# Optimization experiments

Hardware: AMD Instinct MI355X
Metric: run time of the kernel (lower is better)

Reference implementation:

```python
import jax, jax.numpy as jnp
import numpy as np

S, H, E, DFF = 8192, 1024, 8, 4096
CAPACITY = (S * 1) // E  # capacity_factor=1.0, k=1 -> 1024 (>= min_capacity 4)


def setup_inputs() -> dict:
    key = jax.random.key(0)
    ks = jax.random.split(key, 6)
    sc_in = 1.0 / np.sqrt(H)
    sc_ff = 1.0 / np.sqrt(DFF)
    return {
        "hidden_states": jax.random.normal(ks[0], (S, H), dtype=jnp.float32),
        "wg": jax.random.normal(ks[1], (H, E), dtype=jnp.float32) * sc_in,
        "w1": jax.random.normal(ks[2], (E, H, DFF), dtype=jnp.float32) * sc_in,
        "b1": jnp.zeros((E, DFF), dtype=jnp.float32),
        "w2": jax.random.normal(ks[3], (E, DFF, H), dtype=jnp.float32) * sc_ff,
        "b2": jnp.zeros((E, H), dtype=jnp.float32),
    }


def _top1_gate(x, wg):
    # DeepSpeed top1gating (noisy_gate_policy=None, used_token=None)
    logits = x @ wg                                   # [S, E]
    gates = jax.nn.softmax(logits, axis=-1)           # [S, E]
    idx = jnp.argmax(gates, axis=-1)                  # [S]
    mask1 = jax.nn.one_hot(idx, E, dtype=gates.dtype) # [S, E]
    # load-balancing aux loss (uses pre-capacity mask)
    me = jnp.mean(gates, axis=0)
    ce = jnp.mean(mask1, axis=0)
    l_aux = jnp.sum(me * ce) * E
    # capacity-based token dropping
    locations1 = jnp.cumsum(mask1, axis=0) - 1.0      # position within expert
    mask1 = mask1 * (locations1 < CAPACITY)
    exp_counts = jnp.sum(mask1, axis=0).astype(jnp.int32)
    loc_s = jnp.sum(locations1 * mask1, axis=1).astype(jnp.int32)   # [S]
    loc_sc = jax.nn.one_hot(loc_s, CAPACITY, dtype=gates.dtype)     # [S, C]
    combine = jnp.einsum("se,sc->sec", gates * mask1, loc_sc)       # [S, E, C]
    dispatch = (combine > 0).astype(gates.dtype)
    return l_aux, combine, dispatch, exp_counts


def reference(hidden_states, wg, w1, b1, w2, b2):
    l_aux, combine, dispatch, exp_counts = _top1_gate(hidden_states, wg)
    # dispatch tokens to expert slots: [E, C, H]
    disp = jnp.einsum("sec,sh->ech", dispatch, hidden_states)
    # grouped expert FFN (GELU MLP)
    h1 = jax.nn.gelu(jnp.einsum("ech,ehf->ecf", disp, w1) + b1[:, None, :])
    eo = jnp.einsum("ecf,efh->ech", h1, w2) + b2[:, None, :]
    # combine back to token order, weighted by gate values
    out = jnp.einsum("sec,ech->sh", combine, eo)      # [S, H]
    # dropout prob = 0.0 -> identity
    return out, l_aux, exp_counts
```

## Files before the change

### kernel.cpp

```cpp
#include <hip/hip_runtime.h>

#define S_TOK 8192
#define H_DIM 1024
#define NE    8
#define CAP   1024
#define DFF   4096

typedef unsigned short u16;
typedef __bf16 bf16_t;
typedef bf16_t bf16x8 __attribute__((ext_vector_type(8)));
typedef float  f32x4  __attribute__((ext_vector_type(4)));

__device__ __forceinline__ u16 f2bf(float f) {
  union { float f; unsigned u; } a; a.f = f;
  unsigned u = a.u;
  u += 0x7fffu + ((u >> 16) & 1u);
  return (u16)(u >> 16);
}

__device__ __forceinline__ float gelu_tanh(float x) {
  const float c = 0.7978845608028654f;
  float t = tanhf(c * (x + 0.044715f * x * x * x));
  return 0.5f * x * (1.0f + t);
}

__global__ void gate_kernel(const float* __restrict__ x, const float* __restrict__ wg,
                            float* __restrict__ gate, int* __restrict__ expert,
                            int* __restrict__ rank, int* __restrict__ blockCnt,
                            float* __restrict__ blockMe) {
  __shared__ float sg[16][8];
  __shared__ int   se[16];
  int tid = threadIdx.x, lane = tid & 63, w = tid >> 6;
  int b = blockIdx.x;
  for (int j = 0; j < 4; ++j) {
    int t = w * 4 + j;
    int s = b * 16 + t;
    const float* xr = x + (size_t)s * H_DIM;
    float acc[8];
#pragma unroll
    for (int e = 0; e < 8; ++e) acc[e] = 0.f;
#pragma unroll
    for (int i = 0; i < 16; ++i) {
      int h = i * 64 + lane;
      float xv = xr[h];
      float4 wa = *(const float4*)(wg + h * 8);
      float4 wb = *(const float4*)(wg + h * 8 + 4);
      acc[0] += xv * wa.x; acc[1] += xv * wa.y; acc[2] += xv * wa.z; acc[3] += xv * wa.w;
      acc[4] += xv * wb.x; acc[5] += xv * wb.y; acc[6] += xv * wb.z; acc[7] += xv * wb.w;
    }
#pragma unroll
    for (int off = 32; off >= 1; off >>= 1)
#pragma unroll
      for (int e = 0; e < 8; ++e) acc[e] += __shfl_down(acc[e], off);
    if (lane == 0) {
      float mx = acc[0];
#pragma unroll
      for (int e = 1; e < 8; ++e) mx = fmaxf(mx, acc[e]);
      float g[8], Z = 0.f;
#pragma unroll
      for (int e = 0; e < 8; ++e) { g[e] = expf(acc[e] - mx); Z += g[e]; }
      int am = 0; float best = acc[0];
#pragma unroll
      for (int e = 1; e < 8; ++e) if (acc[e] > best) { best = acc[e]; am = e; }
      float inv = 1.f / Z;
#pragma unroll
      for (int e = 0; e < 8; ++e) sg[t][e] = g[e] * inv;
      se[t] = am;
      gate[s] = g[am] * inv;
      expert[s] = am;
    }
  }
  __syncthreads();
  if (tid < 16) {
    int e = se[tid], r = 0;
    for (int t2 = 0; t2 < tid; ++t2) r += (se[t2] == e) ? 1 : 0;
    rank[b * 16 + tid] = r;
  }
  if (tid < 8) {
    int c = 0; float m = 0.f;
#pragma unroll
    for (int t = 0; t < 16; ++t) { c += (se[t] == tid) ? 1 : 0; m += sg[t][tid]; }
    blockCnt[b * 8 + tid] = c;
    blockMe[b * 8 + tid] = m;
  }
}

__global__ void scan_kernel(const int* __restrict__ blockCnt, const float* __restrict__ blockMe,
                            int* __restrict__ blockOff, int* __restrict__ counts,
                            float* __restrict__ tail) {
  int tid = threadIdx.x;
  int e = tid >> 6, lane = tid & 63;
  int run = 0; float msum = 0.f;
  for (int c = 0; c < 8; ++c) {
    int b = c * 64 + lane;
    int v = blockCnt[b * 8 + e];
    float mv = blockMe[b * 8 + e];
    int sc = v;
#pragma unroll
    for (int off = 1; off < 64; off <<= 1) {
      int u = __shfl_up(sc, off);
      if (lane >= off) sc += u;
    }
    blockOff[b * 8 + e] = run + sc - v;
    run += __shfl(sc, 63);
#pragma unroll
    for (int off = 32; off >= 1; off >>= 1) mv += __shfl_down(mv, off);
    msum += __shfl(mv, 0);
  }
  __shared__ float sm[8];
  __shared__ int scnt[8];
  if (lane == 0) {
    sm[e] = msum; scnt[e] = run;
    counts[e] = run < CAP ? run : CAP;
  }
  __syncthreads();
  if (tid == 0) {
    float la = 0.f;
    for (int i = 0; i < 8; ++i)
      la += (sm[i] / (float)S_TOK) * ((float)scnt[i] / (float)S_TOK);
    tail[0] = la * (float)NE;
    for (int i = 0; i < 8; ++i) {
      int cc = scnt[i] < CAP ? scnt[i] : CAP;
      tail[1 + i] = (float)cc;
    }
  }
}

__global__ void assign_kernel(const int* __restrict__ expert, const int* __restrict__ rank,
                              const int* __restrict__ blockOff, int* __restrict__ slot_token) {
  int s = blockIdx.x * 256 + threadIdx.x;
  int e = expert[s];
  int pos = blockOff[(s >> 4) * 8 + e] + rank[s];
  if (pos < CAP) slot_token[e * CAP + pos] = s;
}

__global__ void gather_kernel(const float* __restrict__ x, const int* __restrict__ slot_token,
                              const int* __restrict__ counts, u16* __restrict__ disp) {
  int slot = blockIdx.x;
  int e = slot >> 10, c = slot & 1023;
  int t = threadIdx.x;
  ushort4 v4;
  if (c < counts[e]) {
    int s = slot_token[slot];
    float4 v = *(const float4*)(x + (size_t)s * H_DIM + t * 4);
    v4.x = f2bf(v.x); v4.y = f2bf(v.y); v4.z = f2bf(v.z); v4.w = f2bf(v.w);
  } else {
    v4.x = 0; v4.y = 0; v4.z = 0; v4.w = 0;
  }
  *(ushort4*)(disp + (size_t)slot * H_DIM + t * 4) = v4;
}

__global__ void transpose_convert(const float* __restrict__ src0, u16* __restrict__ dst0,
                                  int R, int C) {
  __shared__ float tile[64][65];
  int e = blockIdx.z;
  const float* src = src0 + (size_t)e * R * C;
  u16* dst = dst0 + (size_t)e * R * C;
  int c0 = blockIdx.x * 64, r0 = blockIdx.y * 64;
  int g = threadIdx.x & 15, rr = threadIdx.x >> 4;
#pragma unroll
  for (int p = 0; p < 4; ++p) {
    int r = rr + p * 16;
    float4 v = *(const float4*)(src + (size_t)(r0 + r) * C + c0 + g * 4);
    tile[r][g * 4 + 0] = v.x;
    tile[r][g * 4 + 1] = v.y;
    tile[r][g * 4 + 2] = v.z;
    tile[r][g * 4 + 3] = v.w;
  }
  __syncthreads();
#pragma unroll
  for (int p = 0; p < 4; ++p) {
    int c = rr + p * 16;
    ushort4 o;
    o.x = f2bf(tile[g * 4 + 0][c]);
    o.y = f2bf(tile[g * 4 + 1][c]);
    o.z = f2bf(tile[g * 4 + 2][c]);
    o.w = f2bf(tile[g * 4 + 3][c]);
    *(ushort4*)(dst + (size_t)(c0 + c) * R + r0 + g * 4) = o;
  }
}

__device__ __forceinline__ void stage_tile(const u16* g, int ldk, u16* lds) {
  int tid = threadIdx.x;
  int lane = tid & 63, w = tid >> 6;
#pragma unroll
  for (int r = 0; r < 2; ++r) {
    int p = (w * 2 + r) * 64 + lane;
    int row = p >> 2;
    int kq = (p & 3) ^ ((row >> 1) & 3);
    const u16* gp = g + (size_t)row * ldk + kq * 8;
    u16* lp = lds + (w * 2 + r) * 512;
    __builtin_amdgcn_global_load_lds((__attribute__((address_space(1))) int*)(gp),
                                     (__attribute__((address_space(3))) int*)(lp),
                                     16, 0, 0);
  }
}

template <int KDIM>
__device__ __forceinline__ void gemm_core(const u16* A, const u16* Bt, int lda, int ldb,
                                          u16* As, u16* Bs, f32x4 acc[4][4]) {
  int tid = threadIdx.x;
  int lane = tid & 63;
  int w = tid >> 6, wm = w >> 1, wn = w & 1;
  int q = lane >> 4, l15 = lane & 15;
  int aoff[4], boff[4];
#pragma unroll
  for (int t = 0; t < 4; ++t) {
    int ra = wm * 64 + t * 16 + l15;
    aoff[t] = ra * 32 + ((q ^ ((ra >> 1) & 3)) * 8);
    int rb = wn * 64 + t * 16 + l15;
    boff[t] = rb * 32 + ((q ^ ((rb >> 1) & 3)) * 8);
  }
  for (int kt = 0; kt < KDIM; kt += 32) {
    stage_tile(A + kt, lda, As);
    stage_tile(Bt + kt, ldb, Bs);
    __syncthreads();
    bf16x8 af[4], bfr[4];
#pragma unroll
    for (int t = 0; t < 4; ++t) af[t] = *(const bf16x8*)(As + aoff[t]);
#pragma unroll
    for (int t = 0; t < 4; ++t) bfr[t] = *(const bf16x8*)(Bs + boff[t]);
#pragma unroll
    for (int mt = 0; mt < 4; ++mt)
#pragma unroll
      for (int nt = 0; nt < 4; ++nt)
        acc[mt][nt] = __builtin_amdgcn_mfma_f32_16x16x32_bf16(af[mt], bfr[nt], acc[mt][nt], 0, 0, 0);
    __syncthreads();
  }
}

__global__ __launch_bounds__(256, 2) void gemm1_kernel(const u16* __restrict__ disp,
                                                       const u16* __restrict__ w1t,
                                                       const float* __restrict__ b1,
                                                       u16* __restrict__ h1) {
  __shared__ __align__(16) u16 As[4096];
  __shared__ __align__(16) u16 Bs[4096];
  int e = blockIdx.z;
  int m0 = blockIdx.y * 128, n0 = blockIdx.x * 128;
  const u16* A  = disp + (size_t)e * CAP * H_DIM + (size_t)m0 * H_DIM;
  const u16* Bt = w1t + (size_t)e * DFF * H_DIM + (size_t)n0 * H_DIM;
  f32x4 acc[4][4];
  f32x4 zero = {0.f, 0.f, 0.f, 0.f};
#pragma unroll
  for (int i = 0; i < 4; ++i)
#pragma unroll
    for (int j = 0; j < 4; ++j) acc[i][j] = zero;
  gemm_core<H_DIM>(A, Bt, H_DIM, H_DIM, As, Bs, acc);
  int tid = threadIdx.x, lane = tid & 63, w = tid >> 6, wm = w >> 1, wn = w & 1;
  int q = lane >> 4, l15 = lane & 15;
  const float* b1e = b1 + e * DFF;
  u16* out = h1 + (size_t)e * CAP * DFF;
#pragma unroll
  for (int mt = 0; mt < 4; ++mt)
#pragma unroll
    for (int nt = 0; nt < 4; ++nt) {
      int col = n0 + wn * 64 + nt * 16 + l15;
      float bias = b1e[col];
#pragma unroll
      for (int r = 0; r < 4; ++r) {
        int row = m0 + wm * 64 + mt * 16 + q * 4 + r;
        out[(size_t)row * DFF + col] = f2bf(gelu_tanh(acc[mt][nt][r] + bias));
      }
    }
}

__global__ __launch_bounds__(512, 4) void gemm2_kernel(const u16* __restrict__ h1,
                                                       const u16* __restrict__ w2t,
                                                       const float* __restrict__ b2,
                                                       const int* __restrict__ slot_token,
                                                       const float* __restrict__ gate,
                                                       const int* __restrict__ counts,
                                                       float* __restrict__ out) {
  __shared__ __align__(16) u16 As[4096];
  __shared__ __align__(16) u16 Bs[4096];
  int e = blockIdx.z;
  int m0 = blockIdx.y * 128, n0 = blockIdx.x * 128;
  const u16* A  = h1 + (size_t)e * CAP * DFF + (size_t)m0 * DFF;
  const u16* Bt = w2t + (size_t)e * H_DIM * DFF + (size_t)n0 * DFF;
  int tid = threadIdx.x, lane = tid & 63, w = tid >> 6;
  int wm = w >> 2, wn = w & 3;
  int q = lane >> 4, l15 = lane & 15;
  f32x4 acc[4][2];
  f32x4 zero = {0.f, 0.f, 0.f, 0.f};
#pragma unroll
  for (int i = 0; i < 4; ++i) { acc[i][0] = zero; acc[i][1] = zero; }

  const u16* gsrc = (w < 4) ? A : Bt;
  u16* ldst = (w < 4) ? As : Bs;
  int q4 = w & 3;
  const u16* gp0[2]; u16* lp[2];
#pragma unroll
  for (int r = 0; r < 2; ++r) {
    int p = (q4 * 2 + r) * 64 + lane;
    int srow = p >> 2;
    int skq = (p & 3) ^ ((srow >> 1) & 3);
    gp0[r] = gsrc + (size_t)srow * DFF + skq * 8;
    lp[r] = ldst + (q4 * 2 + r) * 512;
  }

  int aoff[4], boff[2];
#pragma unroll
  for (int t = 0; t < 4; ++t) {
    int ra = wm * 64 + t * 16 + l15;
    aoff[t] = ra * 32 + ((q ^ ((ra >> 1) & 3)) * 8);
  }
#pragma unroll
  for (int t = 0; t < 2; ++t) {
    int rb = wn * 32 + t * 16 + l15;
    boff[t] = rb * 32 + ((q ^ ((rb >> 1) & 3)) * 8);
  }

  for (int kt = 0; kt < DFF; kt += 32) {
#pragma unroll
    for (int r = 0; r < 2; ++r)
      __builtin_amdgcn_global_load_lds((__attribute__((address_space(1))) int*)(gp0[r] + kt),
                                       (__attribute__((address_space(3))) int*)(lp[r]),
                                       16, 0, 0);
    __syncthreads();
    bf16x8 af[4], bfr[2];
#pragma unroll
    for (int t = 0; t < 4; ++t) af[t] = *(const bf16x8*)(As + aoff[t]);
#pragma unroll
    for (int t = 0; t < 2; ++t) bfr[t] = *(const bf16x8*)(Bs + boff[t]);
#pragma unroll
    for (int mt = 0; mt < 4; ++mt)
#pragma unroll
      for (int nt = 0; nt < 2; ++nt)
        acc[mt][nt] = __builtin_amdgcn_mfma_f32_16x16x32_bf16(af[mt], bfr[nt], acc[mt][nt], 0, 0, 0);
    __syncthreads();
  }

  int cnt = counts[e];
  const float* b2e = b2 + e * H_DIM;
#pragma unroll
  for (int mt = 0; mt < 4; ++mt) {
    int tok[4]; float gv[4];
#pragma unroll
    for (int r = 0; r < 4; ++r) {
      int c = m0 + wm * 64 + mt * 16 + q * 4 + r;
      if (c < cnt) { int s = slot_token[e * CAP + c]; tok[r] = s; gv[r] = gate[s]; }
      else { tok[r] = -1; gv[r] = 0.f; }
    }
#pragma unroll
    for (int nt = 0; nt < 2; ++nt) {
      int col = n0 + wn * 32 + nt * 16 + l15;
      float bias = b2e[col];
#pragma unroll
      for (int r = 0; r < 4; ++r)
        if (tok[r] >= 0)
          out[(size_t)tok[r] * H_DIM + col] = gv[r] * (acc[mt][nt][r] + bias);
    }
  }
}

extern "C" void kernel_launch(void* const* d_in, const int* in_sizes, int n_in,
                              void* d_out, int out_size, void* d_ws, size_t ws_size,
                              hipStream_t stream) {
  const float* x  = (const float*)d_in[0];
  const float* wg = (const float*)d_in[1];
  const float* w1 = (const float*)d_in[2];
  const float* b1 = (const float*)d_in[3];
  const float* w2 = (const float*)d_in[4];
  const float* b2 = (const float*)d_in[5];
  float* out = (float*)d_out;
  char* ws = (char*)d_ws;
  const size_t MB = 1024 * 1024;
  u16* w1t  = (u16*)(ws);
  u16* w2t  = (u16*)(ws + 64 * MB);
  u16* disp = (u16*)(ws + 128 * MB);
  u16* h1   = (u16*)(ws + 144 * MB);
  char* sm = ws + 208 * MB;
  float* gate      = (float*)(sm);
  int*   expert    = (int*)(sm + 32 * 1024);
  int*   rank      = (int*)(sm + 64 * 1024);
  int*   slot_tok  = (int*)(sm + 96 * 1024);
  int*   blockCnt  = (int*)(sm + 128 * 1024);
  int*   blockOff  = (int*)(sm + 144 * 1024);
  float* blockMe   = (float*)(sm + 160 * 1024);
  int*   counts    = (int*)(sm + 176 * 1024);

  hipMemsetAsync(d_out, 0, (size_t)out_size * sizeof(float), stream);
  gate_kernel<<<512, 256, 0, stream>>>(x, wg, gate, expert, rank, blockCnt, blockMe);
  scan_kernel<<<1, 512, 0, stream>>>(blockCnt, blockMe, blockOff, counts,
                                     out + (size_t)S_TOK * H_DIM);
  assign_kernel<<<32, 256, 0, stream>>>(expert, rank, blockOff, slot_tok);
  gather_kernel<<<8192, 256, 0, stream>>>(x, slot_tok, counts, disp);
  transpose_convert<<<dim3(DFF / 64, H_DIM / 64, NE), 256, 0, stream>>>(w1, w1t, H_DIM, DFF);
  transpose_convert<<<dim3(H_DIM / 64, DFF / 64, NE), 256, 0, stream>>>(w2, w2t, DFF, H_DIM);
  gemm1_kernel<<<dim3(DFF / 128, CAP / 128, NE), 256, 0, stream>>>(disp, w1t, b1, h1);
  gemm2_kernel<<<dim3(H_DIM / 128, CAP / 128, NE), 512, 0, stream>>>(h1, w2t, b2,
                                                                     slot_tok, gate, counts, out);
}
```

Measured before the change: 620.8 us.

## Swizzle GEMM block order per XCD, raise occupancy bounds, use exp-based GELU

Both expert GEMMs now launch on a flat 1D grid and remap block indices so that consecutive blocks, which are distributed round-robin across the 8 XCDs, land on the same expert. This keeps each expert's weights and activations local to one XCD's L2. The launch bounds' minimum blocks per CU rise from 2 to 3 for gemm1 and from 4 to 6 for gemm2, which pushes the compiler toward fewer registers and higher occupancy at some risk of spills. GELU-tanh is rewritten in the algebraically equivalent form x*sigmoid(2u) using __expf and a hardware reciprocal, which is cheaper but slightly less precise.

```diff
diff --git a/kernel.cpp b/kernel.cpp
--- a/kernel.cpp
+++ b/kernel.cpp
@@ -18,10 +18,10 @@
   return (u16)(u >> 16);
 }
 
-__device__ __forceinline__ float gelu_tanh(float x) {
-  const float c = 0.7978845608028654f;
-  float t = tanhf(c * (x + 0.044715f * x * x * x));
-  return 0.5f * x * (1.0f + t);
+__device__ __forceinline__ float gelu_fast(float x) {
+  float u = 1.5957691216057308f * x * (1.0f + 0.044715f * x * x);
+  float ez = __expf(-u);
+  return x * __builtin_amdgcn_rcpf(1.0f + ez);
 }
 
 __global__ void gate_kernel(const float* __restrict__ x, const float* __restrict__ wg,
@@ -229,14 +229,19 @@
   }
 }
 
-__global__ __launch_bounds__(256, 2) void gemm1_kernel(const u16* __restrict__ disp,
+__global__ __launch_bounds__(256, 3) void gemm1_kernel(const u16* __restrict__ disp,
                                                        const u16* __restrict__ w1t,
                                                        const float* __restrict__ b1,
                                                        u16* __restrict__ h1) {
   __shared__ __align__(16) u16 As[4096];
   __shared__ __align__(16) u16 Bs[4096];
-  int e = blockIdx.z;
-  int m0 = blockIdx.y * 128, n0 = blockIdx.x * 128;
+  int flat = blockIdx.x;
+  int swz = (flat & 7) * 256 + (flat >> 3);
+  int e  = swz >> 8;
+  int r  = swz & 255;
+  int bx = r >> 3;
+  int by = r & 7;
+  int m0 = by * 128, n0 = bx * 128;
   const u16* A  = disp + (size_t)e * CAP * H_DIM + (size_t)m0 * H_DIM;
   const u16* Bt = w1t + (size_t)e * DFF * H_DIM + (size_t)n0 * H_DIM;
   f32x4 acc[4][4];
@@ -257,14 +262,14 @@
       int col = n0 + wn * 64 + nt * 16 + l15;
       float bias = b1e[col];
 #pragma unroll
-      for (int r = 0; r < 4; ++r) {
-        int row = m0 + wm * 64 + mt * 16 + q * 4 + r;
-        out[(size_t)row * DFF + col] = f2bf(gelu_tanh(acc[mt][nt][r] + bias));
+      for (int rr = 0; rr < 4; ++rr) {
+        int row = m0 + wm * 64 + mt * 16 + q * 4 + rr;
+        out[(size_t)row * DFF + col] = f2bf(gelu_fast(acc[mt][nt][rr] + bias));
       }
     }
 }
 
-__global__ __launch_bounds__(512, 4) void gemm2_kernel(const u16* __restrict__ h1,
+__global__ __launch_bounds__(512, 6) void gemm2_kernel(const u16* __restrict__ h1,
                                                        const u16* __restrict__ w2t,
                                                        const float* __restrict__ b2,
                                                        const int* __restrict__ slot_token,
@@ -273,8 +278,13 @@
                                                        float* __restrict__ out) {
   __shared__ __align__(16) u16 As[4096];
   __shared__ __align__(16) u16 Bs[4096];
-  int e = blockIdx.z;
-  int m0 = blockIdx.y * 128, n0 = blockIdx.x * 128;
+  int flat = blockIdx.x;
+  int swz = (flat & 7) * 64 + (flat >> 3);
+  int e  = swz >> 6;
+  int r  = swz & 63;
+  int bx = r & 7;
+  int by = r >> 3;
+  int m0 = by * 128, n0 = bx * 128;
   const u16* A  = h1 + (size_t)e * CAP * DFF + (size_t)m0 * DFF;
   const u16* Bt = w2t + (size_t)e * H_DIM * DFF + (size_t)n0 * DFF;
   int tid = threadIdx.x, lane = tid & 63, w = tid >> 6;
@@ -290,12 +300,12 @@
   int q4 = w & 3;
   const u16* gp0[2]; u16* lp[2];
 #pragma unroll
-  for (int r = 0; r < 2; ++r) {
-    int p = (q4 * 2 + r) * 64 + lane;
+  for (int r2 = 0; r2 < 2; ++r2) {
+    int p = (q4 * 2 + r2) * 64 + lane;
     int srow = p >> 2;
     int skq = (p & 3) ^ ((srow >> 1) & 3);
-    gp0[r] = gsrc + (size_t)srow * DFF + skq * 8;
-    lp[r] = ldst + (q4 * 2 + r) * 512;
+    gp0[r2] = gsrc + (size_t)srow * DFF + skq * 8;
+    lp[r2] = ldst + (q4 * 2 + r2) * 512;
   }
 
   int aoff[4], boff[2];
@@ -312,9 +322,9 @@
 
   for (int kt = 0; kt < DFF; kt += 32) {
 #pragma unroll
-    for (int r = 0; r < 2; ++r)
-      __builtin_amdgcn_global_load_lds((__attribute__((address_space(1))) int*)(gp0[r] + kt),
-                                       (__attribute__((address_space(3))) int*)(lp[r]),
+    for (int r2 = 0; r2 < 2; ++r2)
+      __builtin_amdgcn_global_load_lds((__attribute__((address_space(1))) int*)(gp0[r2] + kt),
+                                       (__attribute__((address_space(3))) int*)(lp[r2]),
                                        16, 0, 0);
     __syncthreads();
     bf16x8 af[4], bfr[2];
@@ -336,19 +346,19 @@
   for (int mt = 0; mt < 4; ++mt) {
     int tok[4]; float gv[4];
 #pragma unroll
-    for (int r = 0; r < 4; ++r) {
-      int c = m0 + wm * 64 + mt * 16 + q * 4 + r;
-      if (c < cnt) { int s = slot_token[e * CAP + c]; tok[r] = s; gv[r] = gate[s]; }
-      else { tok[r] = -1; gv[r] = 0.f; }
+    for (int rr = 0; rr < 4; ++rr) {
+      int c = m0 + wm * 64 + mt * 16 + q * 4 + rr;
+      if (c < cnt) { int s = slot_token[e * CAP + c]; tok[rr] = s; gv[rr] = gate[s]; }
+      else { tok[rr] = -1; gv[rr] = 0.f; }
     }
 #pragma unroll
     for (int nt = 0; nt < 2; ++nt) {
       int col = n0 + wn * 32 + nt * 16 + l15;
       float bias = b2e[col];
 #pragma unroll
-      for (int r = 0; r < 4; ++r)
-        if (tok[r] >= 0)
-          out[(size_t)tok[r] * H_DIM + col] = gv[r] * (acc[mt][nt][r] + bias);
+      for (int rr = 0; rr < 4; ++rr)
+        if (tok[rr] >= 0)
+          out[(size_t)tok[rr] * H_DIM + col] = gv[rr] * (acc[mt][nt][rr] + bias);
     }
   }
 }
@@ -387,7 +397,6 @@
   gather_kernel<<<8192, 256, 0, stream>>>(x, slot_tok, counts, disp);
   transpose_convert<<<dim3(DFF / 64, H_DIM / 64, NE), 256, 0, stream>>>(w1, w1t, H_DIM, DFF);
   transpose_convert<<<dim3(H_DIM / 64, DFF / 64, NE), 256, 0, stream>>>(w2, w2t, DFF, H_DIM);
-  gemm1_kernel<<<dim3(DFF / 128, CAP / 128, NE), 256, 0, stream>>>(disp, w1t, b1, h1);
-  gemm2_kernel<<<dim3(H_DIM / 128, CAP / 128, NE), 512, 0, stream>>>(h1, w2t, b2,
-                                                                     slot_tok, gate, counts, out);
-}
+  gemm1_kernel<<<2048, 256, 0, stream>>>(disp, w1t, b1, h1);
+  gemm2_kernel<<<512, 512, 0, stream>>>(h1, w2t, b2, slot_tok, gate, counts, out);
+}
```

After: 589.4 us. -5.1%, faster.
